# Performance work log

Measured on AMD Instinct MI355X. Metric: run time of the kernel, lower is better.

The kernel has to match this reference:

```python
import jax, jax.numpy as jnp
import numpy as np

N_NODES = 50000
N_EDGES = 800000
D_IN = 256
D_OUT = 256


def setup_inputs() -> dict:
    key = jax.random.key(0)
    ks = jax.random.split(key, 8)
    x = jax.random.normal(ks[0], (N_NODES, D_IN), dtype=jnp.float32)
    edge_index = jax.random.randint(ks[1], (2, N_EDGES), 0, N_NODES, dtype=jnp.int64)
    W_src = jax.random.normal(ks[2], (D_IN, D_OUT), dtype=jnp.float32) * 0.05
    b_src = jax.random.normal(ks[3], (D_OUT,), dtype=jnp.float32) * 0.05
    W_dst = jax.random.normal(ks[4], (D_IN, D_OUT), dtype=jnp.float32) * 0.05
    b_dst = jax.random.normal(ks[5], (D_OUT,), dtype=jnp.float32) * 0.05
    W_self = jax.random.normal(ks[6], (D_IN, D_OUT), dtype=jnp.float32) * 0.05
    b_self = jax.random.normal(ks[7], (D_OUT,), dtype=jnp.float32) * 0.05
    return {"x": x, "edge_index": edge_index, "W_src": W_src, "b_src": b_src,
            "W_dst": W_dst, "b_dst": b_dst, "W_self": W_self, "b_self": b_self}


def reference(x, edge_index, W_src, b_src, W_dst, b_dst, W_self, b_self):
    # LEConv: messages = src_linear(x[row]) - dst_linear(x[col]);
    # scatter-add messages into destination nodes (col); add self_linear(x).
    # Linear commutes with row-gather, so project once on [N, d] then gather.
    row, col = edge_index[0], edge_index[1]
    src = x @ W_src + b_src            # [N, D_OUT]
    dst = x @ W_dst + b_dst            # [N, D_OUT]
    messages = src[row] - dst[col]     # [E, D_OUT]
    agg = jax.ops.segment_sum(messages, col, num_segments=x.shape[0])  # [N, D_OUT]
    return x @ W_self + b_self + agg
```

## Files before the change

kernel.cpp:

```cpp
#include <hip/hip_runtime.h>

#define D 256

typedef unsigned short ushort_t;
typedef unsigned int uint_t;
typedef __attribute__((ext_vector_type(8))) short short8;
typedef __attribute__((ext_vector_type(4))) float floatx4;

static __device__ __forceinline__ ushort_t f2bf(float f) {
    union { float f; uint_t u; } c; c.f = f;
    uint_t r = (c.u + 0x7FFFu + ((c.u >> 16) & 1u)) >> 16;
    return (ushort_t)r;
}
static __device__ __forceinline__ float bf2f(ushort_t b) {
    union { uint_t u; float f; } c; c.u = ((uint_t)b) << 16;
    return c.f;
}

static __device__ __forceinline__ void async16(const void* g, void* l) {
    __builtin_amdgcn_global_load_lds(
        (const __attribute__((address_space(1))) void*)g,
        (__attribute__((address_space(3))) void*)l, 16, 0, 0);
}

__global__ void prep_kernel(const int* __restrict__ col, int* __restrict__ deg,
                            int* __restrict__ rank,
                            const float* __restrict__ x, ushort_t* __restrict__ xh,
                            const float* __restrict__ Wself, const float* __restrict__ Wsrc,
                            const float* __restrict__ Wdst, ushort_t* __restrict__ BT,
                            int E, int total8, int degB, int cvtB) {
    int b = blockIdx.x;
    if (b < degB) {
        int e = b * 256 + threadIdx.x;
        if (e < E) rank[e] = atomicAdd(&deg[col[e]], 1);
    } else if (b < degB + cvtB) {
        int i = (b - degB) * 256 + threadIdx.x;
        if (i >= total8) return;
        float4 a = ((const float4*)x)[i * 2];
        float4 bb = ((const float4*)x)[i * 2 + 1];
        uint4 o;
        o.x = f2bf(a.x) | ((uint_t)f2bf(a.y) << 16);
        o.y = f2bf(a.z) | ((uint_t)f2bf(a.w) << 16);
        o.z = f2bf(bb.x) | ((uint_t)f2bf(bb.y) << 16);
        o.w = f2bf(bb.z) | ((uint_t)f2bf(bb.w) << 16);
        ((uint4*)xh)[i] = o;
    } else {
        int id = (b - degB - cvtB) * 256 + threadIdx.x;
        if (id >= 256 * 768) return;
        int j = id / 768, k = id % 768;
        float v;
        if (k < 256)      v = Wself[(size_t)k * 256 + j];
        else if (k < 512) v = Wsrc [(size_t)(k - 256) * 256 + j];
        else              v = Wdst [(size_t)(k - 512) * 256 + j];
        BT[id] = f2bf(v);
    }
}

__global__ __launch_bounds__(256) void scanA(const int* __restrict__ deg,
                                             int* __restrict__ off,
                                             int* __restrict__ partials, int n4) {
    __shared__ int wtot[4];
    const int tid = threadIdx.x, lane = tid & 63, wid = tid >> 6;
    int i4 = blockIdx.x * 256 + tid;
    int4 v = (i4 < n4) ? ((const int4*)deg)[i4] : make_int4(0, 0, 0, 0);
    int s = v.x + v.y + v.z + v.w;
    int incl = s;
    #pragma unroll
    for (int st = 1; st < 64; st <<= 1) {
        int t = __shfl_up(incl, st, 64);
        if (lane >= st) incl += t;
    }
    if (lane == 63) wtot[wid] = incl;
    __syncthreads();
    int wbase = 0;
    #pragma unroll
    for (int w = 0; w < 4; ++w) if (w < wid) wbase += wtot[w];
    int excl = incl - s + wbase;
    if (i4 < n4) {
        int4 o;
        o.x = excl; o.y = o.x + v.x; o.z = o.y + v.y; o.w = o.z + v.z;
        ((int4*)off)[i4] = o;
    }
    if (tid == 0) partials[blockIdx.x] = wtot[0] + wtot[1] + wtot[2] + wtot[3];
}

__global__ __launch_bounds__(256) void scanC(int* __restrict__ off,
                                             const int* __restrict__ partials, int n4) {
    __shared__ int base_s;
    const int tid = threadIdx.x;
    if (tid < 64) {
        int v = (tid < blockIdx.x) ? partials[tid] : 0;
        #pragma unroll
        for (int st = 32; st; st >>= 1) v += __shfl_down(v, st, 64);
        if (tid == 0) base_s = v;
    }
    __syncthreads();
    int base = base_s;
    int i4 = blockIdx.x * 256 + tid;
    if (i4 < n4) {
        int4 o = ((int4*)off)[i4];
        o.x += base; o.y += base; o.z += base; o.w += base;
        ((int4*)off)[i4] = o;
    }
}

__global__ void fill_kernel(const int* __restrict__ row, const int* __restrict__ col,
                            const int* __restrict__ rank, const int* __restrict__ off,
                            int* __restrict__ bucket, int E) {
    int e = blockIdx.x * blockDim.x + threadIdx.x;
    if (e >= E) return;
    bucket[off[col[e]] + rank[e]] = row[e];
}

__global__ __launch_bounds__(256) void segsum_kernel(const ushort_t* __restrict__ xh,
                                                     const int* __restrict__ off,
                                                     const int* __restrict__ deg,
                                                     const int* __restrict__ bucket,
                                                     ushort_t* __restrict__ Gh, int N) {
    int node = blockIdx.x * 4 + (threadIdx.x >> 6);
    int lane = threadIdx.x & 63;
    if (node >= N) return;
    int start = off[node];
    int cnt = deg[node];
    float a0 = 0.f, a1 = 0.f, a2 = 0.f, a3 = 0.f;
    int i = 0;
    for (; i + 4 <= cnt; i += 4) {
        int r0 = bucket[start + i];
        int r1 = bucket[start + i + 1];
        int r2 = bucket[start + i + 2];
        int r3 = bucket[start + i + 3];
        ushort4 v0 = ((const ushort4*)(xh + (size_t)r0 * D))[lane];
        ushort4 v1 = ((const ushort4*)(xh + (size_t)r1 * D))[lane];
        ushort4 v2 = ((const ushort4*)(xh + (size_t)r2 * D))[lane];
        ushort4 v3 = ((const ushort4*)(xh + (size_t)r3 * D))[lane];
        a0 += (bf2f(v0.x) + bf2f(v1.x)) + (bf2f(v2.x) + bf2f(v3.x));
        a1 += (bf2f(v0.y) + bf2f(v1.y)) + (bf2f(v2.y) + bf2f(v3.y));
        a2 += (bf2f(v0.z) + bf2f(v1.z)) + (bf2f(v2.z) + bf2f(v3.z));
        a3 += (bf2f(v0.w) + bf2f(v1.w)) + (bf2f(v2.w) + bf2f(v3.w));
    }
    for (; i < cnt; ++i) {
        int r0 = bucket[start + i];
        ushort4 v0 = ((const ushort4*)(xh + (size_t)r0 * D))[lane];
        a0 += bf2f(v0.x); a1 += bf2f(v0.y); a2 += bf2f(v0.z); a3 += bf2f(v0.w);
    }
    ushort4 o;
    o.x = f2bf(a0); o.y = f2bf(a1); o.z = f2bf(a2); o.w = f2bf(a3);
    ((ushort4*)(Gh + (size_t)node * D))[lane] = o;
}

__global__ __launch_bounds__(256, 2) void mfma_gemm(
    const ushort_t* __restrict__ xh, const ushort_t* __restrict__ Gh,
    const ushort_t* __restrict__ BT, const int* __restrict__ deg,
    const float* __restrict__ bsrc, const float* __restrict__ bdst,
    const float* __restrict__ bself, float* __restrict__ out, int N)
{
    __shared__ ushort_t As[8][64][8];
    __shared__ ushort_t Bs[8][64][8];
    __shared__ ushort_t Ds[8][64][8];

    const int tid = threadIdx.x;
    const int lane = tid & 63, wave = tid >> 6;
    const int quad = lane >> 4, l15 = lane & 15;
    const int mg = (wave >> 1) * 4, ng = (wave & 1) * 4;
    const int mbase = blockIdx.x * 128, nbase = blockIdx.y * 128;

    const int ga0 = wave * 2, ga1 = ga0 + 1;
    int ar0 = mbase + ga0 * 16 + l15; if (ar0 >= N) ar0 = N - 1;
    int ar1 = mbase + ga1 * 16 + l15; if (ar1 >= N) ar1 = N - 1;
    const size_t aoff0 = (size_t)ar0 * 256 + quad * 8;
    const size_t aoff1 = (size_t)ar1 * 256 + quad * 8;
    const ushort_t* bp0 = BT + (size_t)(nbase + ga0 * 16 + l15) * 768 + quad * 8;
    const ushort_t* bp1 = BT + (size_t)(nbase + ga1 * 16 + l15) * 768 + quad * 8;

    floatx4 acc1[4][4] = {};
    floatx4 acc2[4][4] = {};

    for (int kt = 0; kt < 16; ++kt) {
        const ushort_t* Asrc = (kt < 8) ? xh : Gh;
        const int ka = (kt & 7) * 32;
        const int kb = kt * 32;
        async16(Asrc + aoff0 + ka, &As[ga0][0][0]);
        async16(Asrc + aoff1 + ka, &As[ga1][0][0]);
        async16(bp0 + kb, &Bs[ga0][0][0]);
        async16(bp1 + kb, &Bs[ga1][0][0]);
        if (kt < 8) {
            async16(bp0 + 512 + kb, &Ds[ga0][0][0]);
            async16(bp1 + 512 + kb, &Ds[ga1][0][0]);
        }
        __syncthreads();

        short8 af[4], bfr[4];
        #pragma unroll
        for (int im = 0; im < 4; ++im)
            af[im] = *(const short8*)(&As[mg + im][lane][0]);
        #pragma unroll
        for (int in = 0; in < 4; ++in)
            bfr[in] = *(const short8*)(&Bs[ng + in][lane][0]);
        #pragma unroll
        for (int im = 0; im < 4; ++im)
            #pragma unroll
            for (int in = 0; in < 4; ++in)
                acc1[im][in] = __builtin_amdgcn_mfma_f32_16x16x32_bf16(
                    af[im], bfr[in], acc1[im][in], 0, 0, 0);
        if (kt < 8) {
            short8 df[4];
            #pragma unroll
            for (int in = 0; in < 4; ++in)
                df[in] = *(const short8*)(&Ds[ng + in][lane][0]);
            #pragma unroll
            for (int im = 0; im < 4; ++im)
                #pragma unroll
                for (int in = 0; in < 4; ++in)
                    acc2[im][in] = __builtin_amdgcn_mfma_f32_16x16x32_bf16(
                        af[im], df[in], acc2[im][in], 0, 0, 0);
        }
        __syncthreads();
    }

    float degv[4][4];
    #pragma unroll
    for (int im = 0; im < 4; ++im)
        #pragma unroll
        for (int r = 0; r < 4; ++r) {
            int gm = mbase + (wave >> 1) * 64 + im * 16 + quad * 4 + r;
            degv[im][r] = (gm < N) ? (float)deg[gm] : 0.f;
        }

    #pragma unroll
    for (int in = 0; in < 4; ++in) {
        int gn = nbase + (wave & 1) * 64 + in * 16 + l15;
        float bs = bself[gn];
        float db = bsrc[gn] - bdst[gn];
        #pragma unroll
        for (int im = 0; im < 4; ++im) {
            #pragma unroll
            for (int r = 0; r < 4; ++r) {
                int gm = mbase + (wave >> 1) * 64 + im * 16 + quad * 4 + r;
                if (gm < N) {
                    float d = degv[im][r];
                    out[(size_t)gm * 256 + gn] =
                        acc1[im][in][r] - d * acc2[im][in][r] + bs + d * db;
                }
            }
        }
    }
}

extern "C" void kernel_launch(void* const* d_in, const int* in_sizes, int n_in,
                              void* d_out, int out_size, void* d_ws, size_t ws_size,
                              hipStream_t stream) {
    const float* x     = (const float*)d_in[0];
    const int*   eidx  = (const int*)d_in[1];
    const float* Wsrc  = (const float*)d_in[2];
    const float* bsrc  = (const float*)d_in[3];
    const float* Wdst  = (const float*)d_in[4];
    const float* bdst  = (const float*)d_in[5];
    const float* Wself = (const float*)d_in[6];
    const float* bself = (const float*)d_in[7];
    float* out = (float*)d_out;

    const int N = in_sizes[0] / D;
    const int E = in_sizes[1] / 2;
    const int* row = eidx;
    const int* col = eidx + E;

    char* p = (char*)d_ws;
    ushort_t* xh  = (ushort_t*)p;        p += (size_t)N * D * sizeof(ushort_t);
    ushort_t* Gh  = (ushort_t*)p;        int* rank = (int*)p;
                                         p += (size_t)N * D * sizeof(ushort_t);
    ushort_t* BT  = (ushort_t*)p;        p += (size_t)768 * 256 * sizeof(ushort_t);
    int* deg      = (int*)p;             p += (size_t)N * sizeof(int);
    int* off      = (int*)p;             p += (size_t)N * sizeof(int);
    int* partials = (int*)p;             p += 64 * sizeof(int);
    int* bucket   = (int*)p;

    hipMemsetAsync(deg, 0, (size_t)N * sizeof(int), stream);

    const int total8 = N * D / 8;
    const int degB = (E + 255) / 256;
    const int cvtB = (total8 + 255) / 256;
    const int btB  = (256 * 768 + 255) / 256;
    prep_kernel<<<degB + cvtB + btB, 256, 0, stream>>>(col, deg, rank, x, xh,
                                                       Wself, Wsrc, Wdst, BT,
                                                       E, total8, degB, cvtB);
    const int n4 = N / 4;
    const int nblk = (n4 + 255) / 256;
    scanA<<<nblk, 256, 0, stream>>>(deg, off, partials, n4);
    scanC<<<nblk, 256, 0, stream>>>(off, partials, n4);
    fill_kernel<<<(E + 255) / 256, 256, 0, stream>>>(row, col, rank, off, bucket, E);
    segsum_kernel<<<(N + 3) / 4, 256, 0, stream>>>(xh, off, deg, bucket, Gh, N);

    dim3 grid((N + 127) / 128, 2);
    mfma_gemm<<<grid, 256, 0, stream>>>(xh, Gh, BT, deg, bsrc, bdst, bself, out, N);
}
```

Before: 281.9 us.

## Fold deg-scaled x into a single K=768 GEMM with full-N tiles and double buffering

Precomputes Zh = deg*x in bf16 inside the scan kernel and negates Wdst in the packed weights, so the output becomes one concatenated GEMM [x|G|Zh]·[Wself;Wsrc;-Wdst] instead of two accumulator sets with a per-row deg combine. The GEMM tile now covers all 256 output columns per block, so A is loaded once instead of twice, and LDS is double-buffered so the next k-tile loads while MFMAs run on the current one. It adds an extra N×D bf16 write and read for Zh and rounds deg*x to bf16 before the GEMM, which may reduce precision. Each block also holds larger accumulators, which may lower occupancy.

Result: no change. 285.7 us (+1.3%).

```diff
diff --git a/kernel.cpp b/kernel.cpp
--- a/kernel.cpp
+++ b/kernel.cpp
@@ -15,6 +15,10 @@
 static __device__ __forceinline__ float bf2f(ushort_t b) {
     union { uint_t u; float f; } c; c.u = ((uint_t)b) << 16;
     return c.f;
+}
+static __device__ __forceinline__ uint_t scale2(uint_t v, float s) {
+    ushort_t lo = (ushort_t)(v & 0xFFFFu), hi = (ushort_t)(v >> 16);
+    return (uint_t)f2bf(bf2f(lo) * s) | ((uint_t)f2bf(bf2f(hi) * s) << 16);
 }
 
 static __device__ __forceinline__ void async16(const void* g, void* l) {
@@ -49,9 +53,9 @@
         if (id >= 256 * 768) return;
         int j = id / 768, k = id % 768;
         float v;
-        if (k < 256)      v = Wself[(size_t)k * 256 + j];
-        else if (k < 512) v = Wsrc [(size_t)(k - 256) * 256 + j];
-        else              v = Wdst [(size_t)(k - 512) * 256 + j];
+        if (k < 256)      v =  Wself[(size_t)k * 256 + j];
+        else if (k < 512) v =  Wsrc [(size_t)(k - 256) * 256 + j];
+        else              v = -Wdst [(size_t)(k - 512) * 256 + j];
         BT[id] = f2bf(v);
     }
 }
@@ -85,22 +89,39 @@
 }
 
 __global__ __launch_bounds__(256) void scanC(int* __restrict__ off,
-                                             const int* __restrict__ partials, int n4) {
-    __shared__ int base_s;
+                                             const int* __restrict__ partials, int n4,
+                                             const ushort_t* __restrict__ xh,
+                                             const int* __restrict__ deg,
+                                             ushort_t* __restrict__ Zh,
+                                             int nblk, int totalChunks) {
     const int tid = threadIdx.x;
-    if (tid < 64) {
-        int v = (tid < blockIdx.x) ? partials[tid] : 0;
-        #pragma unroll
-        for (int st = 32; st; st >>= 1) v += __shfl_down(v, st, 64);
-        if (tid == 0) base_s = v;
-    }
-    __syncthreads();
-    int base = base_s;
-    int i4 = blockIdx.x * 256 + tid;
-    if (i4 < n4) {
-        int4 o = ((int4*)off)[i4];
-        o.x += base; o.y += base; o.z += base; o.w += base;
-        ((int4*)off)[i4] = o;
+    int b = blockIdx.x;
+    if (b < nblk) {
+        __shared__ int base_s;
+        if (tid < 64) {
+            int v = (tid < b) ? partials[tid] : 0;
+            #pragma unroll
+            for (int st = 32; st; st >>= 1) v += __shfl_down(v, st, 64);
+            if (tid == 0) base_s = v;
+        }
+        __syncthreads();
+        int base = base_s;
+        int i4 = b * 256 + tid;
+        if (i4 < n4) {
+            int4 o = ((int4*)off)[i4];
+            o.x += base; o.y += base; o.z += base; o.w += base;
+            ((int4*)off)[i4] = o;
+        }
+    } else {
+        int c = (b - nblk) * 256 + tid;
+        if (c >= totalChunks) return;
+        int node = c >> 5;
+        float s = (float)deg[node];
+        uint4 v = ((const uint4*)xh)[c];
+        uint4 o;
+        o.x = scale2(v.x, s); o.y = scale2(v.y, s);
+        o.z = scale2(v.z, s); o.w = scale2(v.w, s);
+        ((uint4*)Zh)[c] = o;
     }
 }
 
@@ -150,71 +171,72 @@
 
 __global__ __launch_bounds__(256, 2) void mfma_gemm(
     const ushort_t* __restrict__ xh, const ushort_t* __restrict__ Gh,
-    const ushort_t* __restrict__ BT, const int* __restrict__ deg,
+    const ushort_t* __restrict__ Zh, const ushort_t* __restrict__ BT,
+    const int* __restrict__ deg,
     const float* __restrict__ bsrc, const float* __restrict__ bdst,
     const float* __restrict__ bself, float* __restrict__ out, int N)
 {
-    __shared__ ushort_t As[8][64][8];
-    __shared__ ushort_t Bs[8][64][8];
-    __shared__ ushort_t Ds[8][64][8];
+    __shared__ ushort_t As[2][8][64][8];
+    __shared__ ushort_t Bs[2][16][64][8];
 
     const int tid = threadIdx.x;
     const int lane = tid & 63, wave = tid >> 6;
     const int quad = lane >> 4, l15 = lane & 15;
-    const int mg = (wave >> 1) * 4, ng = (wave & 1) * 4;
-    const int mbase = blockIdx.x * 128, nbase = blockIdx.y * 128;
+    const int mhalf = wave >> 1, nhalf = wave & 1;
+    const int mbase = blockIdx.x * 128;
 
     const int ga0 = wave * 2, ga1 = ga0 + 1;
     int ar0 = mbase + ga0 * 16 + l15; if (ar0 >= N) ar0 = N - 1;
     int ar1 = mbase + ga1 * 16 + l15; if (ar1 >= N) ar1 = N - 1;
     const size_t aoff0 = (size_t)ar0 * 256 + quad * 8;
     const size_t aoff1 = (size_t)ar1 * 256 + quad * 8;
-    const ushort_t* bp0 = BT + (size_t)(nbase + ga0 * 16 + l15) * 768 + quad * 8;
-    const ushort_t* bp1 = BT + (size_t)(nbase + ga1 * 16 + l15) * 768 + quad * 8;
-
-    floatx4 acc1[4][4] = {};
-    floatx4 acc2[4][4] = {};
-
-    for (int kt = 0; kt < 16; ++kt) {
-        const ushort_t* Asrc = (kt < 8) ? xh : Gh;
-        const int ka = (kt & 7) * 32;
-        const int kb = kt * 32;
-        async16(Asrc + aoff0 + ka, &As[ga0][0][0]);
-        async16(Asrc + aoff1 + ka, &As[ga1][0][0]);
-        async16(bp0 + kb, &Bs[ga0][0][0]);
-        async16(bp1 + kb, &Bs[ga1][0][0]);
-        if (kt < 8) {
-            async16(bp0 + 512 + kb, &Ds[ga0][0][0]);
-            async16(bp1 + 512 + kb, &Ds[ga1][0][0]);
-        }
+    const ushort_t* bp0 = BT + (size_t)((wave * 4 + 0) * 16 + l15) * 768 + quad * 8;
+    const ushort_t* bp1 = BT + (size_t)((wave * 4 + 1) * 16 + l15) * 768 + quad * 8;
+    const ushort_t* bp2 = BT + (size_t)((wave * 4 + 2) * 16 + l15) * 768 + quad * 8;
+    const ushort_t* bp3 = BT + (size_t)((wave * 4 + 3) * 16 + l15) * 768 + quad * 8;
+    const ushort_t* Asrc_[3] = {xh, Gh, Zh};
+
+    floatx4 acc[4][8] = {};
+
+    async16(xh + aoff0, &As[0][ga0][0][0]);
+    async16(xh + aoff1, &As[0][ga1][0][0]);
+    async16(bp0, &Bs[0][wave * 4 + 0][0][0]);
+    async16(bp1, &Bs[0][wave * 4 + 1][0][0]);
+    async16(bp2, &Bs[0][wave * 4 + 2][0][0]);
+    async16(bp3, &Bs[0][wave * 4 + 3][0][0]);
+
+    for (int kt = 0; kt < 24; ++kt) {
+        const int cur = kt & 1;
         __syncthreads();
-
-        short8 af[4], bfr[4];
+        if (kt < 23) {
+            const int nk = kt + 1, nb = cur ^ 1;
+            const ushort_t* s = Asrc_[nk >> 3];
+            const int ka = (nk & 7) * 32;
+            const int kb = nk * 32;
+            async16(s + aoff0 + ka, &As[nb][ga0][0][0]);
+            async16(s + aoff1 + ka, &As[nb][ga1][0][0]);
+            async16(bp0 + kb, &Bs[nb][wave * 4 + 0][0][0]);
+            async16(bp1 + kb, &Bs[nb][wave * 4 + 1][0][0]);
+            async16(bp2 + kb, &Bs[nb][wave * 4 + 2][0][0]);
+            async16(bp3 + kb, &Bs[nb][wave * 4 + 3][0][0]);
+        }
+        short8 af[4];
         #pragma unroll
         for (int im = 0; im < 4; ++im)
-            af[im] = *(const short8*)(&As[mg + im][lane][0]);
+            af[im] = *(const short8*)(&As[cur][mhalf * 4 + im][lane][0]);
         #pragma unroll
-        for (int in = 0; in < 4; ++in)
-            bfr[in] = *(const short8*)(&Bs[ng + in][lane][0]);
-        #pragma unroll
-        for (int im = 0; im < 4; ++im)
+        for (int h = 0; h < 2; ++h) {
+            short8 bfr[4];
             #pragma unroll
             for (int in = 0; in < 4; ++in)
-                acc1[im][in] = __builtin_amdgcn_mfma_f32_16x16x32_bf16(
-                    af[im], bfr[in], acc1[im][in], 0, 0, 0);
-        if (kt < 8) {
-            short8 df[4];
-            #pragma unroll
-            for (int in = 0; in < 4; ++in)
-                df[in] = *(const short8*)(&Ds[ng + in][lane][0]);
+                bfr[in] = *(const short8*)(&Bs[cur][nhalf * 8 + h * 4 + in][lane][0]);
             #pragma unroll
             for (int im = 0; im < 4; ++im)
                 #pragma unroll
                 for (int in = 0; in < 4; ++in)
-                    acc2[im][in] = __builtin_amdgcn_mfma_f32_16x16x32_bf16(
-                        af[im], df[in], acc2[im][in], 0, 0, 0);
-        }
-        __syncthreads();
+                    acc[im][h * 4 + in] = __builtin_amdgcn_mfma_f32_16x16x32_bf16(
+                        af[im], bfr[in], acc[im][h * 4 + in], 0, 0, 0);
+        }
     }
 
     float degv[4][4];
@@ -222,25 +244,22 @@
     for (int im = 0; im < 4; ++im)
         #pragma unroll
         for (int r = 0; r < 4; ++r) {
-            int gm = mbase + (wave >> 1) * 64 + im * 16 + quad * 4 + r;
+            int gm = mbase + mhalf * 64 + im * 16 + quad * 4 + r;
             degv[im][r] = (gm < N) ? (float)deg[gm] : 0.f;
         }
 
     #pragma unroll
-    for (int in = 0; in < 4; ++in) {
-        int gn = nbase + (wave & 1) * 64 + in * 16 + l15;
+    for (int in = 0; in < 8; ++in) {
+        int gn = nhalf * 128 + in * 16 + l15;
         float bs = bself[gn];
         float db = bsrc[gn] - bdst[gn];
         #pragma unroll
         for (int im = 0; im < 4; ++im) {
             #pragma unroll
             for (int r = 0; r < 4; ++r) {
-                int gm = mbase + (wave >> 1) * 64 + im * 16 + quad * 4 + r;
-                if (gm < N) {
-                    float d = degv[im][r];
-                    out[(size_t)gm * 256 + gn] =
-                        acc1[im][in][r] - d * acc2[im][in][r] + bs + d * db;
-                }
+                int gm = mbase + mhalf * 64 + im * 16 + quad * 4 + r;
+                if (gm < N)
+                    out[(size_t)gm * 256 + gn] = acc[im][in][r] + bs + degv[im][r] * db;
             }
         }
     }
@@ -268,6 +287,7 @@
     ushort_t* xh  = (ushort_t*)p;        p += (size_t)N * D * sizeof(ushort_t);
     ushort_t* Gh  = (ushort_t*)p;        int* rank = (int*)p;
                                          p += (size_t)N * D * sizeof(ushort_t);
+    ushort_t* Zh  = (ushort_t*)p;        p += (size_t)N * D * sizeof(ushort_t);
     ushort_t* BT  = (ushort_t*)p;        p += (size_t)768 * 256 * sizeof(ushort_t);
     int* deg      = (int*)p;             p += (size_t)N * sizeof(int);
     int* off      = (int*)p;             p += (size_t)N * sizeof(int);
@@ -286,10 +306,10 @@
     const int n4 = N / 4;
     const int nblk = (n4 + 255) / 256;
     scanA<<<nblk, 256, 0, stream>>>(deg, off, partials, n4);
-    scanC<<<nblk, 256, 0, stream>>>(off, partials, n4);
+    scanC<<<nblk + cvtB, 256, 0, stream>>>(off, partials, n4, xh, deg, Zh, nblk, total8);
     fill_kernel<<<(E + 255) / 256, 256, 0, stream>>>(row, col, rank, off, bucket, E);
     segsum_kernel<<<(N + 3) / 4, 256, 0, stream>>>(xh, off, deg, bucket, Gh, N);
 
-    dim3 grid((N + 127) / 128, 2);
-    mfma_gemm<<<grid, 256, 0, stream>>>(xh, Gh, BT, deg, bsrc, bdst, bself, out, N);
-}
+    mfma_gemm<<<dim3((N + 127) / 128), 256, 0, stream>>>(
+        xh, Gh, Zh, BT, deg, bsrc, bdst, bself, out, N);
+}
```
